# Kernel tuning notes

Measured on AMD Instinct MI355X. Metric: run time of the kernel, lower is better.

The kernel has to match this reference:

```python
import jax, jax.numpy as jnp
import numpy as np

S, B, F, H, L = 256, 64, 512, 512, 4
INV_SQRT_H = float(1.0 / np.sqrt(H))


def _ln(x, g, b, eps=1e-5):
    # torch nn.LayerNorm: biased variance, eps=1e-5
    mu = jnp.mean(x, axis=-1, keepdims=True)
    var = jnp.var(x, axis=-1, keepdims=True)
    return (x - mu) * jax.lax.rsqrt(var + eps) * g + b


def setup_inputs() -> dict:
    key = jax.random.key(0)
    k1, k2 = jax.random.split(key)
    x = jax.random.normal(k1, (S, B, F), dtype=jnp.float32)  # time-major [S,B,F]
    W = jax.random.normal(k2, (L, 6, F, H), dtype=jnp.float32) * 0.02  # q,k,v,i,f,o
    b = jnp.zeros((L, 6, H), jnp.float32)
    ln_g = jnp.ones((L, 6, H), jnp.float32)
    ln_b = jnp.zeros((L, 6, H), jnp.float32)
    return {"x": x, "W": W, "b": b, "ln_g": ln_g, "ln_b": ln_b}


def reference(x, W, b, ln_g, ln_b):
    # Dropout is identity (eval mode / p effectively 0).
    def step(carry, x_t):
        h, c, n = carry  # each [L,B,H]
        layer_input = x_t  # [B,F]
        hs, cs, ns = [], [], []
        for l in range(L):
            # all 6 gate projections in one einsum: [6,B,H]
            z = jnp.einsum('bf,gfh->gbh', layer_input, W[l]) + b[l][:, None, :]
            z = z.at[1].multiply(INV_SQRT_H)  # k = Wk(x)/sqrt(H) before LN
            z = _ln(z, ln_g[l][:, None, :], ln_b[l][:, None, :])
            q, k, v = z[0], z[1], z[2]
            i = jax.nn.sigmoid(z[3])
            f = jax.nn.sigmoid(z[4])
            o = jax.nn.sigmoid(z[5])
            # (k[:,:,None] @ v[:,None,:]).sum(dim=1) == k.sum(-1,keepdims)*v
            kv_sum = jnp.sum(k, axis=-1, keepdims=True) * v
            c_l = f * c[l] + i * kv_sum
            n_l = f * n[l] + i * k
            n_hat = n_l / (jnp.linalg.norm(n_l, axis=-1, keepdims=True) + 1e-8)
            h_l = o * jnp.tanh(q * n_hat)
            if l > 0:  # residual_conn
                h_l = h_l + layer_input
            layer_input = h_l
            hs.append(h_l); cs.append(c_l); ns.append(n_l)
        h = jnp.stack(hs); c = jnp.stack(cs); n = jnp.stack(ns)
        return (h, c, n), h[-1]

    init = tuple(jnp.zeros((L, B, H), x.dtype) for _ in range(3))
    (h, c, n), out = jax.lax.scan(step, init, x)  # out: [S,B,H] time-major
    return out, h, c, n
```

## Files before the change

### kernel.cpp

```cpp
#include <hip/hip_runtime.h>


typedef unsigned short u16;
typedef unsigned int   u32;
typedef short s8v __attribute__((ext_vector_type(8)));
typedef float f4v __attribute__((ext_vector_type(4)));

#define S_    256
#define B_    64
#define F_    512
#define H_    512
#define L_    4
#define NG    3072
#define RALL  16384
#define CH    16
#define INV_SQRT_H 0.044194173824159216f

__device__ __forceinline__ float bu2f(u16 u) {
    union { u32 i; float f; } z; z.i = ((u32)u) << 16; return z.f;
}
__device__ __forceinline__ u16 f2bf(float f) {
    union { float f; u32 i; } z; z.f = f;
    u32 r = (z.i + 0x7FFFu + ((z.i >> 16) & 1u)) >> 16;
    return (u16)r;
}
__device__ __forceinline__ float sigm(float x)  { return 1.0f / (1.0f + __expf(-x)); }
__device__ __forceinline__ float tanhf_(float x){ return 2.0f / (1.0f + __expf(-2.0f * x)) - 1.0f; }
__device__ __forceinline__ float wred64(float v) {
    #pragma unroll
    for (int m = 1; m < 64; m <<= 1) v += __shfl_xor(v, m);
    return v;
}
__device__ __forceinline__ void gl_lds16(const u16* g, u16* l) {
    __builtin_amdgcn_global_load_lds((const __attribute__((address_space(1))) u32*)g,
                                     (__attribute__((address_space(3))) u32*)l, 16, 0, 0);
}
__device__ __forceinline__ void unp8(uint4 u, float* f) {
    f[0] = bu2f((u16)(u.x & 0xffff)); f[1] = bu2f((u16)(u.x >> 16));
    f[2] = bu2f((u16)(u.y & 0xffff)); f[3] = bu2f((u16)(u.y >> 16));
    f[4] = bu2f((u16)(u.z & 0xffff)); f[5] = bu2f((u16)(u.z >> 16));
    f[6] = bu2f((u16)(u.w & 0xffff)); f[7] = bu2f((u16)(u.w >> 16));
}
__device__ __forceinline__ uint4 pck8(const float* f) {
    uint4 u;
    u.x = (u32)f2bf(f[0]) | ((u32)f2bf(f[1]) << 16);
    u.y = (u32)f2bf(f[2]) | ((u32)f2bf(f[3]) << 16);
    u.z = (u32)f2bf(f[4]) | ((u32)f2bf(f[5]) << 16);
    u.w = (u32)f2bf(f[6]) | ((u32)f2bf(f[7]) << 16);
    return u;
}

__global__ void convw_k(const float* __restrict__ W, u16* __restrict__ WT) {
    __shared__ float tile[32][33];
    const int lg = blockIdx.z;
    const int h0 = blockIdx.x * 32, f0 = blockIdx.y * 32;
    const float* Wb = W  + (size_t)lg * F_ * H_;
    u16*        WTb = WT + (size_t)lg * F_ * H_;
    const int tx = threadIdx.x, ty = threadIdx.y;
    #pragma unroll
    for (int i = 0; i < 32; i += 8)
        tile[ty + i][tx] = Wb[(size_t)(f0 + ty + i) * H_ + h0 + tx];
    __syncthreads();
    #pragma unroll
    for (int i = 0; i < 32; i += 8)
        WTb[(size_t)(h0 + ty + i) * F_ + f0 + tx] = f2bf(tile[tx][ty + i]);
}

__global__ void convx_k(const float* __restrict__ x, u16* __restrict__ A) {
    const int i = blockIdx.x * 256 + threadIdx.x;
    float4 v = ((const float4*)x)[i];
    u32 lo = (u32)f2bf(v.x) | ((u32)f2bf(v.y) << 16);
    u32 hi = (u32)f2bf(v.z) | ((u32)f2bf(v.w) << 16);
    ((uint2*)A)[i] = make_uint2(lo, hi);
}

__global__ __launch_bounds__(256) void gemm_k(const u16* __restrict__ A,
                                              const u16* __restrict__ BT,
                                              u16* __restrict__ Z,
                                              const float* __restrict__ bias,
                                              int arow0) {
    __shared__ u16 lsA[128 * 32];
    __shared__ u16 lsB[128 * 32];
    const int t = threadIdx.x;
    const int ntile = blockIdx.x;
    const int mtile = blockIdx.y;
    const int ncol0 = ntile * 128;
    const u16* Ab = A  + (size_t)(arow0 + mtile * 128) * F_;
    const u16* Bb = BT + (size_t)ntile * 128 * F_;
    const int lane = t & 63, wv = t >> 6;

    f4v acc[4][4];
    #pragma unroll
    for (int i = 0; i < 4; i++)
        #pragma unroll
        for (int j = 0; j < 4; j++) acc[i][j] = 0.0f;

    const int wm = (wv >> 1) * 64, wn = (wv & 1) * 64;
    const int ro = lane & 15, ko = (lane >> 4) * 8;

    for (int kb = 0; kb < 16; ++kb) {
        {
            int c = t, r = c >> 2, kc = c & 3;
            gl_lds16(Ab + (size_t)r * F_ + kb * 32 + kc * 8, lsA + c * 8);
            gl_lds16(Bb + (size_t)r * F_ + kb * 32 + kc * 8, lsB + c * 8);
            c = t + 256; r = c >> 2; kc = c & 3;
            gl_lds16(Ab + (size_t)r * F_ + kb * 32 + kc * 8, lsA + c * 8);
            gl_lds16(Bb + (size_t)r * F_ + kb * 32 + kc * 8, lsB + c * 8);
        }
        __syncthreads();
        s8v fa[4], fb[4];
        #pragma unroll
        for (int i = 0; i < 4; i++) fa[i] = *(const s8v*)(lsA + (wm + i * 16 + ro) * 32 + ko);
        #pragma unroll
        for (int j = 0; j < 4; j++) fb[j] = *(const s8v*)(lsB + (wn + j * 16 + ro) * 32 + ko);
        #pragma unroll
        for (int i = 0; i < 4; i++)
            #pragma unroll
            for (int j = 0; j < 4; j++)
                acc[i][j] = __builtin_amdgcn_mfma_f32_16x16x32_bf16(fa[i], fb[j], acc[i][j], 0, 0, 0);
        __syncthreads();
    }

    const int cl = lane & 15, rq = (lane >> 4) * 4;
    #pragma unroll
    for (int j = 0; j < 4; j++) {
        const int col = ncol0 + wn + j * 16 + cl;
        const float bv = bias[col];
        #pragma unroll
        for (int i = 0; i < 4; i++) {
            const int mbase = mtile * 128 + wm + i * 16 + rq;
            #pragma unroll
            for (int r2 = 0; r2 < 4; r2++)
                Z[(size_t)(mbase + r2) * NG + col] = f2bf(acc[i][j][r2] + bv);
        }
    }
}

__global__ __launch_bounds__(256) void stats_k(const u16* __restrict__ Z,
                                               const float* __restrict__ lng1,
                                               const float* __restrict__ lnb1,
                                               float* __restrict__ stats) {
    const int wid = threadIdx.x >> 6, lane = threadIdx.x & 63;
    const int row = blockIdx.x * 4 + wid;
    const u16* zr = Z + (size_t)row * NG + lane * 8;

    float g1v[8], b1v[8];
    #pragma unroll
    for (int j = 0; j < 8; j++) { g1v[j] = lng1[lane * 8 + j]; b1v[j] = lnb1[lane * 8 + j]; }

    float s[6], sq[6], wk = 0.f, sg1 = 0.f, sb1 = 0.f;
    #pragma unroll
    for (int g = 0; g < 6; ++g) {
        uint4 u = *(const uint4*)(zr + g * 512);
        float f[8];
        unp8(u, f);
        float ls = 0.f, lq = 0.f;
        #pragma unroll
        for (int j = 0; j < 8; j++) { ls += f[j]; lq += f[j] * f[j]; }
        s[g] = ls; sq[g] = lq;
        if (g == 1) {
            #pragma unroll
            for (int j = 0; j < 8; j++) wk += g1v[j] * f[j];
        }
    }
    #pragma unroll
    for (int j = 0; j < 8; j++) { sg1 += g1v[j]; sb1 += b1v[j]; }

    #pragma unroll
    for (int g = 0; g < 6; ++g) { s[g] = wred64(s[g]); sq[g] = wred64(sq[g]); }
    wk = wred64(wk); sg1 = wred64(sg1); sb1 = wred64(sb1);

    if (lane == 0) {
        float* o = stats + (size_t)row * 16;
        const float inv = 1.0f / 512.0f;
        float mu[6], rs[6];
        #pragma unroll
        for (int g = 0; g < 6; ++g) {
            float m = s[g] * inv, e2 = sq[g] * inv;
            if (g == 1) { m *= INV_SQRT_H; e2 *= INV_SQRT_H * INV_SQRT_H; }
            float var = fmaxf(e2 - m * m, 0.0f);
            mu[g] = m; rs[g] = rsqrtf(var + 1e-5f);
        }
        #pragma unroll
        for (int g = 0; g < 6; ++g) { o[g] = mu[g]; o[6 + g] = rs[g]; }
        o[12] = rs[1] * (INV_SQRT_H * wk - mu[1] * sg1) + sb1;
    }
}

__global__ __launch_bounds__(128) void scanA_k(const u16* __restrict__ Z,
                                               const float* __restrict__ stats,
                                               const float* __restrict__ lngl,
                                               const float* __restrict__ lnbl,
                                               u16* __restrict__ nbuf,
                                               u16* __restrict__ pbuf,
                                               float* __restrict__ sumP,
                                               float* __restrict__ sumC,
                                               float* __restrict__ sumN) {
    const int b = blockIdx.y, chunk = blockIdx.z;
    const int h = blockIdx.x * 128 + threadIdx.x;
    __shared__ float sst[CH][16];
    for (int i = threadIdx.x; i < CH * 16; i += 128) {
        const int tc = i >> 4, j = i & 15;
        sst[tc][j] = stats[(size_t)((chunk * CH + tc) * 64 + b) * 16 + j];
    }
    float gg[4], gb[4];
    #pragma unroll
    for (int g = 0; g < 4; ++g) {
        gg[g] = lngl[(g + 1) * 512 + h];
        gb[g] = lnbl[(g + 1) * 512 + h];
    }
    __syncthreads();

    float c = 0.f, n = 0.f, P = 1.f;
    #pragma unroll 4
    for (int tc = 0; tc < CH; ++tc) {
        const int r = (chunk * CH + tc) * 64 + b;
        const u16* zr = Z + (size_t)r * NG + h;
        const float z1 = bu2f(zr[512]);
        const float z2 = bu2f(zr[1024]);
        const float z3 = bu2f(zr[1536]);
        const float z4 = bu2f(zr[2048]);
        const float kk = (z1 * INV_SQRT_H - sst[tc][1]) * sst[tc][7] * gg[0] + gb[0];
        const float vv = (z2 - sst[tc][2]) * sst[tc][8]  * gg[1] + gb[1];
        const float ii = sigm((z3 - sst[tc][3]) * sst[tc][9]  * gg[2] + gb[2]);
        const float ff = sigm((z4 - sst[tc][4]) * sst[tc][10] * gg[3] + gb[3]);
        c = ff * c + ii * (sst[tc][12] * vv);
        n = ff * n + ii * kk;
        P *= ff;
        nbuf[(size_t)r * 512 + h] = f2bf(n);
        pbuf[(size_t)r * 512 + h] = f2bf(P);
    }
    const size_t idx = ((size_t)chunk << 15) + (b << 9) + h;
    sumP[idx] = P; sumC[idx] = c; sumN[idx] = n;
}

__global__ __launch_bounds__(256) void scanB_k(const float* __restrict__ sumP,
                                               const float* __restrict__ sumC,
                                               const float* __restrict__ sumN,
                                               float* __restrict__ n0buf,
                                               float* __restrict__ cstate,
                                               float* __restrict__ nstate,
                                               float* __restrict__ finals,
                                               int t0, int NC, int l) {
    const int idx = blockIdx.x * 256 + threadIdx.x;
    float c, n;
    if (t0 == 0) { c = 0.f; n = 0.f; }
    else { c = cstate[idx]; n = nstate[idx]; }
    for (int ch = 0; ch < NC; ++ch) {
        const size_t o = ((size_t)ch << 15) + idx;
        n0buf[o] = n;
        const float P = sumP[o];
        c = sumC[o] + P * c;
        n = sumN[o] + P * n;
    }
    if (t0 + NC * CH == S_) {
        const int b = idx >> 9, h = idx & 511;
        const size_t so = ((size_t)l * B_ + b) * H_ + h;
        finals[(size_t)L_ * B_ * H_ + so] = c;
        finals[(size_t)2 * L_ * B_ * H_ + so] = n;
    } else {
        cstate[idx] = c; nstate[idx] = n;
    }
}

__global__ __launch_bounds__(256) void normh_k(const u16* __restrict__ Z,
                                               const u16* __restrict__ nbuf,
                                               const u16* __restrict__ pbuf,
                                               const float* __restrict__ n0buf,
                                               const float* __restrict__ stats,
                                               const float* __restrict__ lngl,
                                               const float* __restrict__ lnbl,
                                               float* __restrict__ hbuf,
                                               u16* __restrict__ aoutB,
                                               float* __restrict__ outp,
                                               float* __restrict__ finals,
                                               int t0, int l) {
    const int wid = threadIdx.x >> 6, lane = threadIdx.x & 63;
    const int r = blockIdx.x * 4 + wid;
    const int h0 = lane * 8;

    float nl[8], pv[8];
    unp8(*(const uint4*)(nbuf + (size_t)r * 512 + h0), nl);
    unp8(*(const uint4*)(pbuf + (size_t)r * 512 + h0), pv);
    const float* n0r = n0buf + ((size_t)(r >> 10) << 15) + ((size_t)(r & 63) << 9) + h0;
    const float4 na = *(const float4*)(n0r);
    const float4 nb = *(const float4*)(n0r + 4);
    const float n0v[8] = {na.x, na.y, na.z, na.w, nb.x, nb.y, nb.z, nb.w};

    float nv[8], nsq = 0.f;
    #pragma unroll
    for (int j = 0; j < 8; j++) {
        nv[j] = fmaf(pv[j], n0v[j], nl[j]);
        nsq += nv[j] * nv[j];
    }
    nsq = wred64(nsq);
    const float rinv = 1.0f / (sqrtf(nsq) + 1e-8f);

    const u16* zr = Z + (size_t)r * NG;
    float z0[8], z5[8];
    unp8(*(const uint4*)(zr + h0), z0);
    unp8(*(const uint4*)(zr + 2560 + h0), z5);

    const float* st = stats + (size_t)r * 16;
    const float mu0 = st[0], rs0 = st[6], mu5 = st[5], rs5 = st[11];

    float g0[8], b0[8], g5[8], b5[8];
    #pragma unroll
    for (int j = 0; j < 8; j++) {
        g0[j] = lngl[h0 + j];        b0[j] = lnbl[h0 + j];
        g5[j] = lngl[2560 + h0 + j]; b5[j] = lnbl[2560 + h0 + j];
    }

    const int tl = r >> 6, b = r & 63;
    const int gr = t0 + tl;
    const size_t grow = (((size_t)gr * 64 + b) * 512) + h0;

    float hv[8];
    #pragma unroll
    for (int j = 0; j < 8; j++) {
        const float q  = (z0[j] - mu0) * rs0 * g0[j] + b0[j];
        const float oo = sigm((z5[j] - mu5) * rs5 * g5[j] + b5[j]);
        hv[j] = oo * tanhf_(q * nv[j] * rinv);
    }
    if (l > 0) {
        #pragma unroll
        for (int j = 0; j < 8; j++) hv[j] += hbuf[grow + j];
    }
    if (outp) {
        #pragma unroll
        for (int j = 0; j < 8; j++) outp[grow + j] = hv[j];
    } else {
        #pragma unroll
        for (int j = 0; j < 8; j++) hbuf[grow + j] = hv[j];
    }
    if (aoutB) *(uint4*)(aoutB + grow) = pck8(hv);

    if (gr == S_ - 1) {
        const size_t so = (((size_t)l * B_ + b) * 512) + h0;
        #pragma unroll
        for (int j = 0; j < 8; j++) finals[so + j] = hv[j];
    }
}

extern "C" void kernel_launch(void* const* d_in, const int* in_sizes, int n_in,
                              void* d_out, int out_size, void* d_ws, size_t ws_size,
                              hipStream_t stream) {
    const float* x   = (const float*)d_in[0];
    const float* W   = (const float*)d_in[1];
    const float* bia = (const float*)d_in[2];
    const float* lng = (const float*)d_in[3];
    const float* lnb = (const float*)d_in[4];
    float* out = (float*)d_out;

    const size_t WT_B = (size_t)L_ * 6 * H_ * F_ * 2;
    const size_t A_B  = (size_t)RALL * F_ * 2;
    const size_t ST_B = (size_t)RALL * 16 * 4;
    const size_t CS_B = (size_t)B_ * H_ * 4;
    const size_t HB_B = (size_t)RALL * H_ * 4;
    auto zB  = [](int T) { return (size_t)T * B_ * NG * 2; };
    auto nB  = [](int T) { return (size_t)T * B_ * H_ * 2; };
    auto cxB = [](int T) { return (size_t)(T / CH) * B_ * H_ * 4; };
    const size_t base = WT_B + A_B + ST_B + 2 * CS_B + HB_B + 32768;

    int T = 16;
    const int cand[3] = {256, 64, 16};
    for (int i = 0; i < 3; i++) {
        const int Tc = cand[i];
        if (ws_size >= base + zB(Tc) + 2 * nB(Tc) + 4 * cxB(Tc)) { T = Tc; break; }
    }
    const int NC = T / CH;

    char* ws = (char*)d_ws;
    size_t off = 0;
    auto take = [&](size_t nb) { size_t o = off; off += (nb + 255) & ~(size_t)255; return o; };
    u16*   WT    = (u16*)  (ws + take(WT_B));
    u16*   Abf   = (u16*)  (ws + take(A_B));
    float* stats = (float*)(ws + take(ST_B));
    float* cs    = (float*)(ws + take(CS_B));
    float* ns    = (float*)(ws + take(CS_B));
    float* hbuf  = (float*)(ws + take(HB_B));
    u16*   zb    = (u16*)  (ws + take(zB(T)));
    u16*   nbuf  = (u16*)  (ws + take(nB(T)));
    u16*   pbuf  = (u16*)  (ws + take(nB(T)));
    float* sumP  = (float*)(ws + take(cxB(T)));
    float* sumC  = (float*)(ws + take(cxB(T)));
    float* sumN  = (float*)(ws + take(cxB(T)));
    float* n0buf = (float*)(ws + take(cxB(T)));

    convw_k<<<dim3(16, 16, 24), dim3(32, 8), 0, stream>>>(W, WT);
    convx_k<<<dim3(RALL * F_ / 4 / 256), dim3(256), 0, stream>>>(x, Abf);

    float* finals = out + (size_t)S_ * B_ * H_;
    for (int l = 0; l < L_; ++l) {
        const u16*   WTl   = WT  + (size_t)l * 6 * H_ * F_;
        const float* biasl = bia + (size_t)l * NG;
        const float* lngl  = lng + (size_t)l * 6 * H_;
        const float* lnbl  = lnb + (size_t)l * 6 * H_;
        for (int j = 0; j < S_ / T; ++j) {
            const int t0 = j * T, arow0 = t0 * B_;
            const int rows = T * B_;
            gemm_k<<<dim3(24, rows / 128), dim3(256), 0, stream>>>(Abf, WTl, zb, biasl, arow0);
            stats_k<<<dim3(rows / 4), dim3(256), 0, stream>>>(zb, lngl + H_, lnbl + H_, stats);
            scanA_k<<<dim3(4, B_, NC), dim3(128), 0, stream>>>(zb, stats, lngl, lnbl,
                                                               nbuf, pbuf, sumP, sumC, sumN);
            scanB_k<<<dim3(128), dim3(256), 0, stream>>>(sumP, sumC, sumN, n0buf,
                                                         cs, ns, finals, t0, NC, l);
            normh_k<<<dim3(rows / 4), dim3(256), 0, stream>>>(zb, nbuf, pbuf, n0buf, stats,
                                                              lngl, lnbl, hbuf,
                                                              (l < 3) ? Abf : (u16*)nullptr,
                                                              (l == 3) ? out : (float*)nullptr,
                                                              finals, t0, l);
        }
    }
}
```

Measured before the change: 671.5 us.

## Fuse LayerNorm row statistics into GEMM epilogue and swizzle LDS tiles

The GEMM epilogue now computes per-row partial sums, sums of squares and the gamma-weighted k sum from fp32 accumulators. These are reduced across lanes and through shared memory and written as per-tile partials. A small stats2 kernel combines them, replacing the stats kernel that re-read the whole bf16 Z buffer. The LDS loads also get an XOR swizzle on the k-chunk to cut bank conflicts, and the sums of gamma/beta are precomputed once per layer. Statistics now come from fp32 values instead of bf16-rounded ones, which slightly changes numerics, and the epilogue gains shuffle and shared-memory work.

```diff
diff --git a/kernel.cpp b/kernel.cpp
--- a/kernel.cpp
+++ b/kernel.cpp
@@ -74,13 +74,30 @@
     ((uint2*)A)[i] = make_uint2(lo, hi);
 }
 
+__global__ void sumgb_k(const float* __restrict__ lng, const float* __restrict__ lnb,
+                        float* __restrict__ sgb) {
+    const int l = blockIdx.x, lane = threadIdx.x;
+    float s = 0.f, b = 0.f;
+    #pragma unroll
+    for (int j = 0; j < 8; j++) {
+        s += lng[(size_t)l * 6 * 512 + 512 + j * 64 + lane];
+        b += lnb[(size_t)l * 6 * 512 + 512 + j * 64 + lane];
+    }
+    s = wred64(s); b = wred64(b);
+    if (lane == 0) { sgb[l * 2] = s; sgb[l * 2 + 1] = b; }
+}
+
 __global__ __launch_bounds__(256) void gemm_k(const u16* __restrict__ A,
                                               const u16* __restrict__ BT,
                                               u16* __restrict__ Z,
                                               const float* __restrict__ bias,
+                                              const float* __restrict__ lng1,
+                                              float2* __restrict__ spart,
+                                              float* __restrict__ wkpart,
                                               int arow0) {
     __shared__ u16 lsA[128 * 32];
     __shared__ u16 lsB[128 * 32];
+    __shared__ float sred[128][2][3];
     const int t = threadIdx.x;
     const int ntile = blockIdx.x;
     const int mtile = blockIdx.y;
@@ -96,23 +113,23 @@
         for (int j = 0; j < 4; j++) acc[i][j] = 0.0f;
 
     const int wm = (wv >> 1) * 64, wn = (wv & 1) * 64;
-    const int ro = lane & 15, ko = (lane >> 4) * 8;
+    const int ro = lane & 15, kq = lane >> 4;
+    const int swz = ((ro >> 1) & 3) ^ kq;
+
+    const int r0 = t >> 2,          kc0 = (t & 3)         ^ ((r0 >> 1) & 3);
+    const int r1 = (t + 256) >> 2,  kc1 = ((t + 256) & 3) ^ ((r1 >> 1) & 3);
 
     for (int kb = 0; kb < 16; ++kb) {
-        {
-            int c = t, r = c >> 2, kc = c & 3;
-            gl_lds16(Ab + (size_t)r * F_ + kb * 32 + kc * 8, lsA + c * 8);
-            gl_lds16(Bb + (size_t)r * F_ + kb * 32 + kc * 8, lsB + c * 8);
-            c = t + 256; r = c >> 2; kc = c & 3;
-            gl_lds16(Ab + (size_t)r * F_ + kb * 32 + kc * 8, lsA + c * 8);
-            gl_lds16(Bb + (size_t)r * F_ + kb * 32 + kc * 8, lsB + c * 8);
-        }
+        gl_lds16(Ab + (size_t)r0 * F_ + kb * 32 + kc0 * 8, lsA + t * 8);
+        gl_lds16(Bb + (size_t)r0 * F_ + kb * 32 + kc0 * 8, lsB + t * 8);
+        gl_lds16(Ab + (size_t)r1 * F_ + kb * 32 + kc1 * 8, lsA + (t + 256) * 8);
+        gl_lds16(Bb + (size_t)r1 * F_ + kb * 32 + kc1 * 8, lsB + (t + 256) * 8);
         __syncthreads();
         s8v fa[4], fb[4];
         #pragma unroll
-        for (int i = 0; i < 4; i++) fa[i] = *(const s8v*)(lsA + (wm + i * 16 + ro) * 32 + ko);
-        #pragma unroll
-        for (int j = 0; j < 4; j++) fb[j] = *(const s8v*)(lsB + (wn + j * 16 + ro) * 32 + ko);
+        for (int i = 0; i < 4; i++) fa[i] = *(const s8v*)(lsA + (wm + i * 16 + ro) * 32 + swz * 8);
+        #pragma unroll
+        for (int j = 0; j < 4; j++) fb[j] = *(const s8v*)(lsB + (wn + j * 16 + ro) * 32 + swz * 8);
         #pragma unroll
         for (int i = 0; i < 4; i++)
             #pragma unroll
@@ -121,70 +138,78 @@
         __syncthreads();
     }
 
-    const int cl = lane & 15, rq = (lane >> 4) * 4;
-    #pragma unroll
-    for (int j = 0; j < 4; j++) {
-        const int col = ncol0 + wn + j * 16 + cl;
-        const float bv = bias[col];
-        #pragma unroll
-        for (int i = 0; i < 4; i++) {
-            const int mbase = mtile * 128 + wm + i * 16 + rq;
+    const int cl = lane & 15, rq = kq * 4;
+    const int gate = ncol0 >> 9;
+    float g1v[4] = {0.f, 0.f, 0.f, 0.f};
+    if (gate == 1) {
+        #pragma unroll
+        for (int j = 0; j < 4; j++) g1v[j] = lng1[ncol0 - 512 + wn + j * 16 + cl];
+    }
+    #pragma unroll
+    for (int i = 0; i < 4; i++) {
+        float sv[4] = {0, 0, 0, 0}, qv[4] = {0, 0, 0, 0}, wvv[4] = {0, 0, 0, 0};
+        const int mbase = mtile * 128 + wm + i * 16 + rq;
+        #pragma unroll
+        for (int j = 0; j < 4; j++) {
+            const int col = ncol0 + wn + j * 16 + cl;
+            const float bv = bias[col];
             #pragma unroll
-            for (int r2 = 0; r2 < 4; r2++)
-                Z[(size_t)(mbase + r2) * NG + col] = f2bf(acc[i][j][r2] + bv);
+            for (int r2 = 0; r2 < 4; r2++) {
+                const float v = acc[i][j][r2] + bv;
+                Z[(size_t)(mbase + r2) * NG + col] = f2bf(v);
+                sv[r2] += v; qv[r2] += v * v;
+                if (gate == 1) wvv[r2] += g1v[j] * v;
+            }
         }
-    }
-}
-
-__global__ __launch_bounds__(256) void stats_k(const u16* __restrict__ Z,
-                                               const float* __restrict__ lng1,
-                                               const float* __restrict__ lnb1,
-                                               float* __restrict__ stats) {
-    const int wid = threadIdx.x >> 6, lane = threadIdx.x & 63;
-    const int row = blockIdx.x * 4 + wid;
-    const u16* zr = Z + (size_t)row * NG + lane * 8;
-
-    float g1v[8], b1v[8];
-    #pragma unroll
-    for (int j = 0; j < 8; j++) { g1v[j] = lng1[lane * 8 + j]; b1v[j] = lnb1[lane * 8 + j]; }
-
-    float s[6], sq[6], wk = 0.f, sg1 = 0.f, sb1 = 0.f;
+        #pragma unroll
+        for (int r2 = 0; r2 < 4; r2++) {
+            #pragma unroll
+            for (int m = 1; m < 16; m <<= 1) {
+                sv[r2]  += __shfl_xor(sv[r2], m);
+                qv[r2]  += __shfl_xor(qv[r2], m);
+                if (gate == 1) wvv[r2] += __shfl_xor(wvv[r2], m);
+            }
+            if (cl == 0) {
+                const int rl = wm + i * 16 + rq + r2;
+                sred[rl][wn >> 6][0] = sv[r2];
+                sred[rl][wn >> 6][1] = qv[r2];
+                sred[rl][wn >> 6][2] = (gate == 1) ? wvv[r2] : 0.f;
+            }
+        }
+    }
+    __syncthreads();
+    if (t < 128) {
+        const int row = mtile * 128 + t;
+        spart[(size_t)row * 24 + ntile] =
+            make_float2(sred[t][0][0] + sred[t][1][0], sred[t][0][1] + sred[t][1][1]);
+        if (gate == 1)
+            wkpart[(size_t)row * 4 + (ntile - 4)] = sred[t][0][2] + sred[t][1][2];
+    }
+}
+
+__global__ __launch_bounds__(256) void stats2_k(const float2* __restrict__ spart,
+                                                const float* __restrict__ wkpart,
+                                                const float* __restrict__ sgb,
+                                                float* __restrict__ stats) {
+    const int row = blockIdx.x * 256 + threadIdx.x;
+    const float2* sp = spart + (size_t)row * 24;
+    float* o = stats + (size_t)row * 16;
+    const float inv = 1.0f / 512.0f;
+    float mu1 = 0.f, rs1 = 0.f;
     #pragma unroll
     for (int g = 0; g < 6; ++g) {
-        uint4 u = *(const uint4*)(zr + g * 512);
-        float f[8];
-        unp8(u, f);
-        float ls = 0.f, lq = 0.f;
-        #pragma unroll
-        for (int j = 0; j < 8; j++) { ls += f[j]; lq += f[j] * f[j]; }
-        s[g] = ls; sq[g] = lq;
-        if (g == 1) {
-            #pragma unroll
-            for (int j = 0; j < 8; j++) wk += g1v[j] * f[j];
-        }
-    }
-    #pragma unroll
-    for (int j = 0; j < 8; j++) { sg1 += g1v[j]; sb1 += b1v[j]; }
-
-    #pragma unroll
-    for (int g = 0; g < 6; ++g) { s[g] = wred64(s[g]); sq[g] = wred64(sq[g]); }
-    wk = wred64(wk); sg1 = wred64(sg1); sb1 = wred64(sb1);
-
-    if (lane == 0) {
-        float* o = stats + (size_t)row * 16;
-        const float inv = 1.0f / 512.0f;
-        float mu[6], rs[6];
-        #pragma unroll
-        for (int g = 0; g < 6; ++g) {
-            float m = s[g] * inv, e2 = sq[g] * inv;
-            if (g == 1) { m *= INV_SQRT_H; e2 *= INV_SQRT_H * INV_SQRT_H; }
-            float var = fmaxf(e2 - m * m, 0.0f);
-            mu[g] = m; rs[g] = rsqrtf(var + 1e-5f);
-        }
-        #pragma unroll
-        for (int g = 0; g < 6; ++g) { o[g] = mu[g]; o[6 + g] = rs[g]; }
-        o[12] = rs[1] * (INV_SQRT_H * wk - mu[1] * sg1) + sb1;
-    }
+        float ss = 0.f, qq = 0.f;
+        #pragma unroll
+        for (int u = 0; u < 4; u++) { const float2 v = sp[g * 4 + u]; ss += v.x; qq += v.y; }
+        float m = ss * inv, e2 = qq * inv;
+        if (g == 1) { m *= INV_SQRT_H; e2 *= INV_SQRT_H * INV_SQRT_H; }
+        const float rs = rsqrtf(fmaxf(e2 - m * m, 0.0f) + 1e-5f);
+        o[g] = m; o[6 + g] = rs;
+        if (g == 1) { mu1 = m; rs1 = rs; }
+    }
+    const float wk = wkpart[(size_t)row * 4] + wkpart[(size_t)row * 4 + 1] +
+                     wkpart[(size_t)row * 4 + 2] + wkpart[(size_t)row * 4 + 3];
+    o[12] = rs1 * (INV_SQRT_H * wk - mu1 * sgb[0]) + sgb[1];
 }
 
 __global__ __launch_bounds__(128) void scanA_k(const u16* __restrict__ Z,
@@ -355,12 +380,14 @@
     const size_t WT_B = (size_t)L_ * 6 * H_ * F_ * 2;
     const size_t A_B  = (size_t)RALL * F_ * 2;
     const size_t ST_B = (size_t)RALL * 16 * 4;
+    const size_t SP_B = (size_t)RALL * 24 * 8;
+    const size_t WK_B = (size_t)RALL * 4 * 4;
     const size_t CS_B = (size_t)B_ * H_ * 4;
     const size_t HB_B = (size_t)RALL * H_ * 4;
     auto zB  = [](int T) { return (size_t)T * B_ * NG * 2; };
     auto nB  = [](int T) { return (size_t)T * B_ * H_ * 2; };
     auto cxB = [](int T) { return (size_t)(T / CH) * B_ * H_ * 4; };
-    const size_t base = WT_B + A_B + ST_B + 2 * CS_B + HB_B + 32768;
+    const size_t base = WT_B + A_B + ST_B + SP_B + WK_B + 2 * CS_B + HB_B + 65536;
 
     int T = 16;
     const int cand[3] = {256, 64, 16};
@@ -376,6 +403,9 @@
     u16*   WT    = (u16*)  (ws + take(WT_B));
     u16*   Abf   = (u16*)  (ws + take(A_B));
     float* stats = (float*)(ws + take(ST_B));
+    float2* spart= (float2*)(ws + take(SP_B));
+    float* wkprt = (float*)(ws + take(WK_B));
+    float* sgb   = (float*)(ws + take(256));
     float* cs    = (float*)(ws + take(CS_B));
     float* ns    = (float*)(ws + take(CS_B));
     float* hbuf  = (float*)(ws + take(HB_B));
@@ -389,6 +419,7 @@
 
     convw_k<<<dim3(16, 16, 24), dim3(32, 8), 0, stream>>>(W, WT);
     convx_k<<<dim3(RALL * F_ / 4 / 256), dim3(256), 0, stream>>>(x, Abf);
+    sumgb_k<<<dim3(L_), dim3(64), 0, stream>>>(lng, lnb, sgb);
 
     float* finals = out + (size_t)S_ * B_ * H_;
     for (int l = 0; l < L_; ++l) {
@@ -399,8 +430,9 @@
         for (int j = 0; j < S_ / T; ++j) {
             const int t0 = j * T, arow0 = t0 * B_;
             const int rows = T * B_;
-            gemm_k<<<dim3(24, rows / 128), dim3(256), 0, stream>>>(Abf, WTl, zb, biasl, arow0);
-            stats_k<<<dim3(rows / 4), dim3(256), 0, stream>>>(zb, lngl + H_, lnbl + H_, stats);
+            gemm_k<<<dim3(24, rows / 128), dim3(256), 0, stream>>>(Abf, WTl, zb, biasl,
+                                                                   lngl + H_, spart, wkprt, arow0);
+            stats2_k<<<dim3(rows / 256), dim3(256), 0, stream>>>(spart, wkprt, sgb + l * 2, stats);
             scanA_k<<<dim3(4, B_, NC), dim3(128), 0, stream>>>(zb, stats, lngl, lnbl,
                                                                nbuf, pbuf, sumP, sumC, sumN);
             scanB_k<<<dim3(128), dim3(256), 0, stream>>>(sumP, sumC, sumN, n0buf,
```

After: 807.7 us. 1.2x slower.
